# Kernel optimization log

Hardware: AMD Instinct MI355X
Metric: run time of the kernel (lower is better)

Reference implementation:

```python
import jax, jax.numpy as jnp
import numpy as np

N_NODES = 20000
N_EDGES = 320000
IN_CH = 256
HID = 128
HEADS = 4
OUT_CH = 200
NUM_GRAPHS = 64
NEG_SLOPE = 0.2


def setup_inputs() -> dict:
    key = jax.random.key(0)
    ks = jax.random.split(key, 16)
    x = jax.random.normal(ks[0], (N_NODES, IN_CH), dtype=jnp.float32)
    edge_index = jax.random.randint(ks[1], (2, N_EDGES), 0, N_NODES, dtype=jnp.int64)
    batch = jnp.sort(jax.random.randint(ks[2], (N_NODES,), 0, NUM_GRAPHS, dtype=jnp.int64))

    def lin(k, fan_in, fan_out):
        return jax.random.normal(k, (fan_in, fan_out), dtype=jnp.float32) / np.sqrt(fan_in)

    def att(k, h, c):
        return jax.random.normal(k, (h, c), dtype=jnp.float32) / np.sqrt(c)

    return {
        "x": x, "edge_index": edge_index, "batch": batch,
        "W1": lin(ks[3], IN_CH, HEADS * HID),
        "a_src1": att(ks[4], HEADS, HID), "a_dst1": att(ks[5], HEADS, HID),
        "b1": jnp.zeros((HEADS * HID,), jnp.float32),
        "W2": lin(ks[6], HEADS * HID, HEADS * HID),
        "a_src2": att(ks[7], HEADS, HID), "a_dst2": att(ks[8], HEADS, HID),
        "b2": jnp.zeros((HEADS * HID,), jnp.float32),
        "W3": lin(ks[9], HEADS * HID, HID),
        "a_src3": att(ks[10], 1, HID), "a_dst3": att(ks[11], 1, HID),
        "b3": jnp.zeros((HID,), jnp.float32),
        "fc_w": lin(ks[12], HID, OUT_CH),
        "fc_b": jnp.zeros((OUT_CH,), jnp.float32),
    }


def gat_conv(x, src, dst, W, a_src, a_dst, bias):
    """PyG GATConv (concat=True, negative_slope=0.2, self-loops appended by caller)."""
    N = x.shape[0]
    heads, out_ch = a_src.shape
    h = (x @ W).reshape(N, heads, out_ch)                 # [N,H,C]
    alpha_s = jnp.einsum('nhc,hc->nh', h, a_src)          # [N,H]
    alpha_d = jnp.einsum('nhc,hc->nh', h, a_dst)
    e = jax.nn.leaky_relu(alpha_s[src] + alpha_d[dst], NEG_SLOPE)  # [E,H]
    # segment softmax over edges sharing the same target node
    m = jax.ops.segment_max(e, dst, num_segments=N)
    e = jnp.exp(e - m[dst])
    denom = jax.ops.segment_sum(e, dst, num_segments=N)
    alpha = e / (denom[dst] + 1e-16)                      # [E,H]
    msg = h[src] * alpha[:, :, None]                      # [E,H,C]
    out = jax.ops.segment_sum(msg, dst, num_segments=N)   # [N,H,C]
    return out.reshape(N, heads * out_ch) + bias


def reference(x, edge_index, batch, W1, a_src1, a_dst1, b1,
              W2, a_src2, a_dst2, b2, W3, a_src3, a_dst3, b3, fc_w, fc_b):
    N = x.shape[0]
    loop = jnp.arange(N, dtype=edge_index.dtype)
    src = jnp.concatenate([edge_index[0], loop])
    dst = jnp.concatenate([edge_index[1], loop])

    h = jax.nn.elu(gat_conv(x, src, dst, W1, a_src1, a_dst1, b1))
    h = jax.nn.elu(gat_conv(h, src, dst, W2, a_src2, a_dst2, b2))
    h = jax.nn.elu(gat_conv(h, src, dst, W3, a_src3, a_dst3, b3))

    # global_mean_pool over graph ids
    sums = jax.ops.segment_sum(h, batch, num_segments=NUM_GRAPHS)
    cnts = jax.ops.segment_sum(jnp.ones((N,), h.dtype), batch, num_segments=NUM_GRAPHS)
    pooled = sums / jnp.maximum(cnts, 1.0)[:, None]       # [G,HID]
    # F.dropout with training=False is identity
    logits = pooled @ fc_w + fc_b                          # [G,OUT_CH]
    return logits
```

## Files before the change

### kernel.cpp

```cpp
#include <hip/hip_runtime.h>
#include <hip/hip_bf16.h>
#include <stdint.h>

#define N_NODES   20000
#define N_EDGES   320000
#define E_TOT     (N_EDGES + N_NODES)
#define IN_CH     256
#define HID       128
#define HEADS     4
#define OUT_CH    200
#define NUM_GRAPHS 64
#define M_PAD     20096

typedef __bf16 bf16_t;
typedef __bf16 bf16x8 __attribute__((ext_vector_type(8)));
typedef __bf16 bf16x2 __attribute__((ext_vector_type(2)));
typedef float  f32x4  __attribute__((ext_vector_type(4)));

__device__ __forceinline__ bool detect_bf16(const unsigned short* __restrict__ xu16) {
  int lane = threadIdx.x & 63;
  unsigned short v = xu16[2 * lane];
  int e = (v >> 7) & 0xff;
  unsigned long long b = __ballot(e >= 90 && e <= 160);
  return __popcll(b) >= 40;
}
__device__ __forceinline__ bool detect_i64(const unsigned* __restrict__ eidx) {
  int lane = threadIdx.x & 63;
  unsigned long long b = __ballot(eidx[2 * lane + 1] == 0u);
  return __popcll(b) >= 32;
}

struct SmallCvt {
  const void* src[11];
  bf16_t* dst[11];
  int n[11];
};

__global__ void prep(const void* __restrict__ W1, const void* __restrict__ W2,
                     const void* __restrict__ W3, bf16_t* __restrict__ W1T,
                     bf16_t* __restrict__ W2T, bf16_t* __restrict__ W3T,
                     SmallCvt tab, const unsigned short* __restrict__ xu16,
                     const int* __restrict__ eidx, const int* __restrict__ batch,
                     int* __restrict__ esrc, int* __restrict__ edst,
                     int* __restrict__ b32, int* __restrict__ deg) {
  bool isbf = detect_bf16(xu16);
  bool i64  = detect_i64((const unsigned*)eidx);
  int i = blockIdx.x * 256 + threadIdx.x;
  if (i < N_EDGES) {
    int s = i64 ? eidx[2 * i] : eidx[i];
    int d = i64 ? eidx[2 * (N_EDGES + i)] : eidx[N_EDGES + i];
    esrc[i] = s;
    edst[i] = d;
    atomicAdd(&deg[d], 1);
  }
  if (i < N_NODES) {
    b32[i] = i64 ? batch[2 * i] : batch[i];
    atomicAdd(&deg[i], 1);
  }
  if (i < 131072) {
    int k = i >> 9, nn = i & 511;
    bf16_t v = isbf ? ((const bf16_t*)W1)[i] : (bf16_t)((const float*)W1)[i];
    W1T[(size_t)nn * 256 + k] = v;
  } else if (i < 131072 + 262144) {
    int i2 = i - 131072;
    int k = i2 >> 9, nn = i2 & 511;
    bf16_t v = isbf ? ((const bf16_t*)W2)[i2] : (bf16_t)((const float*)W2)[i2];
    W2T[(size_t)nn * 512 + k] = v;
  } else if (i < 131072 + 262144 + 65536) {
    int i3 = i - 131072 - 262144;
    int k = i3 >> 7, nn = i3 & 127;
    bf16_t v = isbf ? ((const bf16_t*)W3)[i3] : (bf16_t)((const float*)W3)[i3];
    W3T[(size_t)nn * 512 + k] = v;
  } else {
    int j = i - 458752;
    for (int s = 0; s < 11; ++s) {
      if (j < tab.n[s]) {
        tab.dst[s][j] = isbf ? ((const bf16_t*)tab.src[s])[j]
                             : (bf16_t)((const float*)tab.src[s])[j];
        break;
      }
      j -= tab.n[s];
    }
  }
}

__launch_bounds__(1024)
__global__ void scan_deg_block(const int* __restrict__ deg, int* __restrict__ off,
                               int* __restrict__ cursor) {
  const int PT = 20;
  int t = threadIdx.x;
  int lane = t & 63, wid = t >> 6;
  int base = t * PT;
  int v[PT];
  int s = 0;
#pragma unroll
  for (int j = 0; j < PT; ++j) {
    int i = base + j;
    v[j] = (i < N_NODES) ? deg[i] : 0;
    s += v[j];
  }
  int x = s;
  for (int d = 1; d < 64; d <<= 1) {
    int y = __shfl_up(x, d);
    if (lane >= d) x += y;
  }
  __shared__ int wsum[16];
  if (lane == 63) wsum[wid] = x;
  __syncthreads();
  if (t < 16) {
    int y = wsum[t];
    for (int d = 1; d < 16; d <<= 1) {
      int z = __shfl_up(y, d);
      if (t >= d) y += z;
    }
    wsum[t] = y;
  }
  __syncthreads();
  int run = (wid > 0 ? wsum[wid - 1] : 0) + (x - s);
#pragma unroll
  for (int j = 0; j < PT; ++j) {
    int i = base + j;
    if (i < N_NODES) { off[i] = run; cursor[i] = 0; run += v[j]; }
  }
  if (t == 1023) off[N_NODES] = run;
}

__global__ void scatter_kernel(const int* __restrict__ esrc, const int* __restrict__ edst,
                               const int* __restrict__ off, int* __restrict__ cursor,
                               int* __restrict__ csr_src) {
  int e = blockIdx.x * 256 + threadIdx.x;
  if (e >= E_TOT) return;
  int s, d;
  if (e < N_EDGES) { s = esrc[e]; d = edst[e]; } else { s = d = e - N_EDGES; }
  int pos = off[d] + atomicAdd(&cursor[d], 1);
  csr_src[pos] = s;
}

template<bool MAYBE_F32>
__launch_bounds__(256)
__global__ void gemm_bf16(const void* __restrict__ Av, const bf16_t* __restrict__ BT,
                          bf16_t* __restrict__ C, int M, int N, int K,
                          const bf16_t* __restrict__ a_src, const bf16_t* __restrict__ a_dst,
                          float* __restrict__ as, float* __restrict__ ad, int H) {
  bool isbf = MAYBE_F32 ? detect_bf16((const unsigned short*)Av) : true;
  const bf16_t* A  = (const bf16_t*)Av;
  const float*  Af = (const float*)Av;
  __shared__ bf16_t As[128 * 32];
  __shared__ bf16_t Bs[128 * 32];
  __shared__ float sred[2][128];
  __shared__ float dred[2][128];
  const int tid  = threadIdx.x;
  const int lane = tid & 63;
  const int w    = tid >> 6;
  const int wm   = w & 1, wn = w >> 1;
  const int bm   = blockIdx.x * 128;
  const int bn   = blockIdx.y * 128;
  const int quad = lane >> 4;
  const int l16  = lane & 15;
  const int hd   = bn >> 7;

  f32x4 zero = {0.f, 0.f, 0.f, 0.f};
  f32x4 acc[4][4];
  for (int i = 0; i < 4; ++i)
    for (int j = 0; j < 4; ++j) acc[i][j] = zero;

  const int c0 = tid, c1 = tid + 256;
  const int r0 = c0 >> 2, s0 = c0 & 3;
  const int r1 = c1 >> 2, s1 = c1 & 3;
  int ga0 = bm + r0; if (ga0 > M - 1) ga0 = M - 1;
  int ga1 = bm + r1; if (ga1 > M - 1) ga1 = M - 1;

  for (int k0 = 0; k0 < K; k0 += 32) {
    if (!MAYBE_F32 || isbf) {
      __syncthreads();
      __builtin_amdgcn_global_load_lds(
          (const __attribute__((address_space(1))) void*)(A + (size_t)ga0 * K + k0 + s0 * 8),
          (__attribute__((address_space(3))) void*)(As + (size_t)(w * 64) * 8), 16, 0, 0);
      __builtin_amdgcn_global_load_lds(
          (const __attribute__((address_space(1))) void*)(BT + (size_t)(bn + r0) * K + k0 + s0 * 8),
          (__attribute__((address_space(3))) void*)(Bs + (size_t)(w * 64) * 8), 16, 0, 0);
      __builtin_amdgcn_global_load_lds(
          (const __attribute__((address_space(1))) void*)(A + (size_t)ga1 * K + k0 + s1 * 8),
          (__attribute__((address_space(3))) void*)(As + (size_t)(256 + w * 64) * 8), 16, 0, 0);
      __builtin_amdgcn_global_load_lds(
          (const __attribute__((address_space(1))) void*)(BT + (size_t)(bn + r1) * K + k0 + s1 * 8),
          (__attribute__((address_space(3))) void*)(Bs + (size_t)(256 + w * 64) * 8), 16, 0, 0);
      __syncthreads();
    } else {
      bf16x8 va0, va1;
      const float* p0 = Af + (size_t)ga0 * K + k0 + s0 * 8;
      const float* p1 = Af + (size_t)ga1 * K + k0 + s1 * 8;
      f32x4 l0 = *(const f32x4*)p0, h0 = *(const f32x4*)(p0 + 4);
      f32x4 l1 = *(const f32x4*)p1, h1 = *(const f32x4*)(p1 + 4);
      for (int j = 0; j < 4; ++j) {
        va0[j] = (bf16_t)l0[j]; va0[j + 4] = (bf16_t)h0[j];
        va1[j] = (bf16_t)l1[j]; va1[j + 4] = (bf16_t)h1[j];
      }
      bf16x8 vb0 = *(const bf16x8*)(BT + (size_t)(bn + r0) * K + k0 + s0 * 8);
      bf16x8 vb1 = *(const bf16x8*)(BT + (size_t)(bn + r1) * K + k0 + s1 * 8);
      __syncthreads();
      *(bf16x8*)(As + c0 * 8) = va0;
      *(bf16x8*)(Bs + c0 * 8) = vb0;
      *(bf16x8*)(As + c1 * 8) = va1;
      *(bf16x8*)(Bs + c1 * 8) = vb1;
      __syncthreads();
    }

    bf16x8 af[4], bfr[4];
    for (int mt = 0; mt < 4; ++mt) {
      int m_local = wm * 64 + mt * 16 + l16;
      af[mt] = *(const bf16x8*)(As + m_local * 32 + quad * 8);
    }
    for (int nt = 0; nt < 4; ++nt) {
      int n_local = wn * 64 + nt * 16 + l16;
      bfr[nt] = *(const bf16x8*)(Bs + n_local * 32 + quad * 8);
    }
    for (int mt = 0; mt < 4; ++mt)
      for (int nt = 0; nt < 4; ++nt)
        acc[mt][nt] = __builtin_amdgcn_mfma_f32_16x16x32_bf16(af[mt], bfr[nt], acc[mt][nt], 0, 0, 0);
  }

  for (int mt = 0; mt < 4; ++mt) {
    for (int r = 0; r < 4; ++r) {
      int m = bm + wm * 64 + mt * 16 + quad * 4 + r;
      if (m >= M) continue;
      for (int nt = 0; nt < 4; ++nt) {
        int n = bn + wn * 64 + nt * 16 + l16;
        C[(size_t)m * N + n] = (bf16_t)acc[mt][nt][r];
      }
    }
  }

  float av[4], dv[4];
  for (int nt = 0; nt < 4; ++nt) {
    int ch = wn * 64 + nt * 16 + l16;
    av[nt] = (float)a_src[hd * 128 + ch];
    dv[nt] = (float)a_dst[hd * 128 + ch];
  }
  for (int mt = 0; mt < 4; ++mt) {
    for (int r = 0; r < 4; ++r) {
      float s = acc[mt][0][r] * av[0] + acc[mt][1][r] * av[1]
              + acc[mt][2][r] * av[2] + acc[mt][3][r] * av[3];
      float d = acc[mt][0][r] * dv[0] + acc[mt][1][r] * dv[1]
              + acc[mt][2][r] * dv[2] + acc[mt][3][r] * dv[3];
      for (int o = 1; o < 16; o <<= 1) {
        s += __shfl_xor(s, o);
        d += __shfl_xor(d, o);
      }
      if (l16 == 0) {
        int row_local = wm * 64 + mt * 16 + quad * 4 + r;
        sred[wn][row_local] = s;
        dred[wn][row_local] = d;
      }
    }
  }
  __syncthreads();
  if (tid < 128) {
    int m = bm + tid;
    if (m < M) {
      as[m * H + hd] = sred[0][tid] + sred[1][tid];
      ad[m * H + hd] = dred[0][tid] + dred[1][tid];
    }
  }
}

template<int CPL>
__launch_bounds__(256)
__global__ void agg_fused(const bf16_t* __restrict__ h, const int* __restrict__ off,
                          const int* __restrict__ csr_src, const float* __restrict__ as,
                          const float* __restrict__ ad, const bf16_t* __restrict__ bias,
                          bf16_t* __restrict__ outp, int H) {
  typedef __bf16 vec_t __attribute__((ext_vector_type(CPL)));
  const int C = CPL * 64;
  int lane = threadIdx.x & 63;
  int n = blockIdx.x * 4 + (threadIdx.x >> 6);
  if (n >= N_NODES) return;
  int start = __builtin_amdgcn_readfirstlane(off[n]);
  int end   = __builtin_amdgcn_readfirstlane(off[n + 1]);
  int c0 = lane * CPL;
  int hd = c0 >> 7;
  float adv = ad[n * H + hd];
  float acc[CPL];
  for (int j = 0; j < CPL; ++j) acc[j] = 0.f;
  float den = 0.f;

  int pos = start;
  for (; pos + 3 < end; pos += 4) {
    int s0 = __builtin_amdgcn_readfirstlane(csr_src[pos]);
    int s1 = __builtin_amdgcn_readfirstlane(csr_src[pos + 1]);
    int s2 = __builtin_amdgcn_readfirstlane(csr_src[pos + 2]);
    int s3 = __builtin_amdgcn_readfirstlane(csr_src[pos + 3]);
    vec_t hv0 = *(const vec_t*)(h + (size_t)s0 * C + c0);
    vec_t hv1 = *(const vec_t*)(h + (size_t)s1 * C + c0);
    vec_t hv2 = *(const vec_t*)(h + (size_t)s2 * C + c0);
    vec_t hv3 = *(const vec_t*)(h + (size_t)s3 * C + c0);
    float e0 = as[s0 * H + hd] + adv; e0 = e0 > 0.f ? e0 : 0.2f * e0;
    float e1 = as[s1 * H + hd] + adv; e1 = e1 > 0.f ? e1 : 0.2f * e1;
    float e2 = as[s2 * H + hd] + adv; e2 = e2 > 0.f ? e2 : 0.2f * e2;
    float e3 = as[s3 * H + hd] + adv; e3 = e3 > 0.f ? e3 : 0.2f * e3;
    float w0 = __expf(e0), w1 = __expf(e1), w2 = __expf(e2), w3 = __expf(e3);
    den += (w0 + w1) + (w2 + w3);
    for (int j = 0; j < CPL; ++j)
      acc[j] += (w0 * (float)hv0[j] + w1 * (float)hv1[j])
              + (w2 * (float)hv2[j] + w3 * (float)hv3[j]);
  }
  for (; pos < end; ++pos) {
    int s0 = __builtin_amdgcn_readfirstlane(csr_src[pos]);
    vec_t hv0 = *(const vec_t*)(h + (size_t)s0 * C + c0);
    float e0 = as[s0 * H + hd] + adv; e0 = e0 > 0.f ? e0 : 0.2f * e0;
    float w0 = __expf(e0);
    den += w0;
    for (int j = 0; j < CPL; ++j) acc[j] += w0 * (float)hv0[j];
  }

  float inv = 1.f / (den + 1e-16f);
  vec_t ov;
  for (int j = 0; j < CPL; ++j) {
    float o = acc[j] * inv + (float)bias[c0 + j];
    o = o > 0.f ? o : expm1f(o);
    ov[j] = (bf16_t)o;
  }
  *(vec_t*)(outp + (size_t)n * C + c0) = ov;
}

__launch_bounds__(256)
__global__ void pool_fc2(const bf16_t* __restrict__ h3, const int* __restrict__ batch,
                         const bf16_t* __restrict__ fcw, const bf16_t* __restrict__ fcb,
                         void* __restrict__ outp, const unsigned short* __restrict__ xu16) {
  bool isbf = detect_bf16(xu16);
  int g = blockIdx.x;
  int lo = 0, hi = N_NODES;
  while (lo < hi) { int mid = (lo + hi) >> 1; if (batch[mid] < g) lo = mid + 1; else hi = mid; }
  int start = lo;
  hi = N_NODES;
  while (lo < hi) { int mid = (lo + hi) >> 1; if (batch[mid] < g + 1) lo = mid + 1; else hi = mid; }
  int end = lo, cnt = end - start;

  int t = threadIdx.x;
  int wave = t >> 6, lane = t & 63;
  int c0 = lane * 2;
  float a0 = 0.f, a1 = 0.f;
  for (int n = start + wave; n < end; n += 4) {
    bf16x2 v = *(const bf16x2*)(h3 + (size_t)n * HID + c0);
    a0 += (float)v[0];
    a1 += (float)v[1];
  }
  __shared__ float red[4][HID];
  red[wave][c0] = a0;
  red[wave][c0 + 1] = a1;
  __syncthreads();
  __shared__ float pooled[HID];
  if (t < HID) {
    float s = red[0][t] + red[1][t] + red[2][t] + red[3][t];
    pooled[t] = s / (float)(cnt > 0 ? cnt : 1);
  }
  __syncthreads();
  if (t < OUT_CH) {
    float a = (float)fcb[t];
    for (int c = 0; c < HID; ++c) a += pooled[c] * (float)fcw[c * OUT_CH + t];
    if (isbf) ((bf16_t*)outp)[g * OUT_CH + t] = (bf16_t)a;
    else      ((float*)outp)[g * OUT_CH + t] = a;
  }
}

extern "C" void kernel_launch(void* const* d_in, const int* in_sizes, int n_in,
                              void* d_out, int out_size, void* d_ws, size_t ws_size,
                              hipStream_t stream) {
  const void* x    = d_in[0];
  const void* eidx = d_in[1];
  const void* batch= d_in[2];
  const void* W1   = d_in[3];
  const void* a_s1 = d_in[4];
  const void* a_d1 = d_in[5];
  const void* b1   = d_in[6];
  const void* W2   = d_in[7];
  const void* a_s2 = d_in[8];
  const void* a_d2 = d_in[9];
  const void* b2   = d_in[10];
  const void* W3   = d_in[11];
  const void* a_s3 = d_in[12];
  const void* a_d3 = d_in[13];
  const void* b3   = d_in[14];
  const void* fcw  = d_in[15];
  const void* fcb  = d_in[16];
  const unsigned short* xu16 = (const unsigned short*)x;

  char* p = (char*)d_ws;
  auto carve = [&](size_t nbytes) { char* r = p; p += (nbytes + 255) & ~(size_t)255; return r; };
  bf16_t*   W1T    = (bf16_t*)carve((size_t)512 * 256 * 2);
  bf16_t*   W2T    = (bf16_t*)carve((size_t)512 * 512 * 2);
  bf16_t*   W3T    = (bf16_t*)carve((size_t)128 * 512 * 2);
  bf16_t*   hA     = (bf16_t*)carve((size_t)M_PAD * 512 * 2);
  bf16_t*   hB     = (bf16_t*)carve((size_t)M_PAD * 512 * 2);
  bf16_t*   sm     = (bf16_t*)carve((size_t)32768 * 2);
  bf16_t *as1b = sm, *ad1b = sm + 512, *b1b = sm + 1024,
         *as2b = sm + 1536, *ad2b = sm + 2048, *b2b = sm + 2560,
         *as3b = sm + 3072, *ad3b = sm + 3200, *b3b = sm + 3328,
         *fcwb = sm + 3456, *fcbb = sm + 29056;
  float*    asb    = (float*)carve((size_t)N_NODES * 4 * 4);
  float*    adb    = (float*)carve((size_t)N_NODES * 4 * 4);
  int*      deg    = (int*)carve((size_t)N_NODES * 4);
  int*      off    = (int*)carve((size_t)(N_NODES + 1) * 4);
  int*      cursor = (int*)carve((size_t)N_NODES * 4);
  int*      csr_src= (int*)carve((size_t)E_TOT * 4);
  int*      esrc32 = (int*)carve((size_t)N_EDGES * 4);
  int*      edst32 = (int*)carve((size_t)N_EDGES * 4);
  int*      bat32  = (int*)carve((size_t)N_NODES * 4);

  dim3 b256(256);
  const int NG4 = (N_NODES + 3) / 4;

  SmallCvt tab;
  const void* srcs[11] = {a_s1, a_d1, b1, a_s2, a_d2, b2, a_s3, a_d3, b3, fcw, fcb};
  bf16_t* dsts[11] = {as1b, ad1b, b1b, as2b, ad2b, b2b, as3b, ad3b, b3b, fcwb, fcbb};
  int ns[11] = {512, 512, 512, 512, 512, 512, 128, 128, 128, 25600, 200};
  for (int i = 0; i < 11; ++i) { tab.src[i] = srcs[i]; tab.dst[i] = dsts[i]; tab.n[i] = ns[i]; }

  hipMemsetAsync(deg, 0, (size_t)N_NODES * 4, stream);
  prep<<<dim3((458752 + 29256 + 255) / 256), b256, 0, stream>>>(
      W1, W2, W3, W1T, W2T, W3T, tab, xu16,
      (const int*)eidx, (const int*)batch, esrc32, edst32, bat32, deg);

  scan_deg_block<<<dim3(1), dim3(1024), 0, stream>>>(deg, off, cursor);
  scatter_kernel<<<dim3((E_TOT + 255) / 256), b256, 0, stream>>>(esrc32, edst32, off, cursor, csr_src);

  gemm_bf16<true><<<dim3(157, 4), b256, 0, stream>>>(x, W1T, hA, N_NODES, 512, 256,
                                                     as1b, ad1b, asb, adb, 4);
  agg_fused<8><<<dim3(NG4), b256, 0, stream>>>(hA, off, csr_src, asb, adb, b1b, hB, 4);

  gemm_bf16<false><<<dim3(157, 4), b256, 0, stream>>>(hB, W2T, hA, N_NODES, 512, 512,
                                                      as2b, ad2b, asb, adb, 4);
  agg_fused<8><<<dim3(NG4), b256, 0, stream>>>(hA, off, csr_src, asb, adb, b2b, hB, 4);

  gemm_bf16<false><<<dim3(157, 1), b256, 0, stream>>>(hB, W3T, hA, N_NODES, 128, 512,
                                                      as3b, ad3b, asb, adb, 1);
  agg_fused<2><<<dim3(NG4), b256, 0, stream>>>(hA, off, csr_src, asb, adb, b3b, hB, 1);

  pool_fc2<<<dim3(NUM_GRAPHS), b256, 0, stream>>>(hB, bat32, fcwb, fcbb, d_out, xu16);
}
```

Measured before the change: 370.8 us.

## Split GAT aggregation into 64-channel slices with two edges per wave

Replaces the per-node aggregation kernel, where one wave covered the whole feature row with 8 channels per lane, with a sliced kernel. Each block now handles one 64-channel slice for four nodes, and each wave splits its lanes into two halves that process alternating edges; the halves are combined with a cross-half shuffle before the output is written. The aim is more parallelism and fewer registers per thread. In exchange, the neighbor index and attention-score loads and the exp are repeated once per slice, the per-lane loads shrink to 4 bytes, and the 4-edge unrolling is gone.

```diff
diff --git a/kernel.cpp b/kernel.cpp
--- a/kernel.cpp
+++ b/kernel.cpp
@@ -264,63 +264,53 @@
   }
 }
 
-template<int CPL>
+template<int C, int SLICES>
 __launch_bounds__(256)
-__global__ void agg_fused(const bf16_t* __restrict__ h, const int* __restrict__ off,
-                          const int* __restrict__ csr_src, const float* __restrict__ as,
-                          const float* __restrict__ ad, const bf16_t* __restrict__ bias,
-                          bf16_t* __restrict__ outp, int H) {
-  typedef __bf16 vec_t __attribute__((ext_vector_type(CPL)));
-  const int C = CPL * 64;
+__global__ void agg_sliced(const bf16_t* __restrict__ h, const int* __restrict__ off,
+                           const int* __restrict__ csr_src, const float* __restrict__ as,
+                           const float* __restrict__ ad, const bf16_t* __restrict__ bias,
+                           bf16_t* __restrict__ outp, int H) {
+  int slice = blockIdx.x % SLICES;
+  int grp   = blockIdx.x / SLICES;
+  int wave  = threadIdx.x >> 6;
+  int n = grp * 4 + wave;
+  if (n >= N_NODES) return;
   int lane = threadIdx.x & 63;
-  int n = blockIdx.x * 4 + (threadIdx.x >> 6);
-  if (n >= N_NODES) return;
+  int half = lane >> 5;
+  int l32  = lane & 31;
+  int cbase = slice * 64;
+  int hd = cbase >> 7;
+  int c = cbase + l32 * 2;
   int start = __builtin_amdgcn_readfirstlane(off[n]);
   int end   = __builtin_amdgcn_readfirstlane(off[n + 1]);
-  int c0 = lane * CPL;
-  int hd = c0 >> 7;
   float adv = ad[n * H + hd];
-  float acc[CPL];
-  for (int j = 0; j < CPL; ++j) acc[j] = 0.f;
-  float den = 0.f;
-
-  int pos = start;
-  for (; pos + 3 < end; pos += 4) {
-    int s0 = __builtin_amdgcn_readfirstlane(csr_src[pos]);
-    int s1 = __builtin_amdgcn_readfirstlane(csr_src[pos + 1]);
-    int s2 = __builtin_amdgcn_readfirstlane(csr_src[pos + 2]);
-    int s3 = __builtin_amdgcn_readfirstlane(csr_src[pos + 3]);
-    vec_t hv0 = *(const vec_t*)(h + (size_t)s0 * C + c0);
-    vec_t hv1 = *(const vec_t*)(h + (size_t)s1 * C + c0);
-    vec_t hv2 = *(const vec_t*)(h + (size_t)s2 * C + c0);
-    vec_t hv3 = *(const vec_t*)(h + (size_t)s3 * C + c0);
-    float e0 = as[s0 * H + hd] + adv; e0 = e0 > 0.f ? e0 : 0.2f * e0;
-    float e1 = as[s1 * H + hd] + adv; e1 = e1 > 0.f ? e1 : 0.2f * e1;
-    float e2 = as[s2 * H + hd] + adv; e2 = e2 > 0.f ? e2 : 0.2f * e2;
-    float e3 = as[s3 * H + hd] + adv; e3 = e3 > 0.f ? e3 : 0.2f * e3;
-    float w0 = __expf(e0), w1 = __expf(e1), w2 = __expf(e2), w3 = __expf(e3);
-    den += (w0 + w1) + (w2 + w3);
-    for (int j = 0; j < CPL; ++j)
-      acc[j] += (w0 * (float)hv0[j] + w1 * (float)hv1[j])
-              + (w2 * (float)hv2[j] + w3 * (float)hv3[j]);
-  }
-  for (; pos < end; ++pos) {
-    int s0 = __builtin_amdgcn_readfirstlane(csr_src[pos]);
-    vec_t hv0 = *(const vec_t*)(h + (size_t)s0 * C + c0);
-    float e0 = as[s0 * H + hd] + adv; e0 = e0 > 0.f ? e0 : 0.2f * e0;
-    float w0 = __expf(e0);
-    den += w0;
-    for (int j = 0; j < CPL; ++j) acc[j] += w0 * (float)hv0[j];
-  }
-
-  float inv = 1.f / (den + 1e-16f);
-  vec_t ov;
-  for (int j = 0; j < CPL; ++j) {
-    float o = acc[j] * inv + (float)bias[c0 + j];
-    o = o > 0.f ? o : expm1f(o);
-    ov[j] = (bf16_t)o;
-  }
-  *(vec_t*)(outp + (size_t)n * C + c0) = ov;
+  float a0 = 0.f, a1 = 0.f, den = 0.f;
+
+  for (int pos = start; pos < end; pos += 2) {
+    int p = pos + half;
+    bool valid = p < end;
+    int pc = valid ? p : end - 1;
+    int src = csr_src[pc];
+    float e = as[src * H + hd] + adv;
+    e = e > 0.f ? e : 0.2f * e;
+    float wgt = valid ? __expf(e) : 0.f;
+    bf16x2 hv = *(const bf16x2*)(h + (size_t)src * C + c);
+    a0 += wgt * (float)hv[0];
+    a1 += wgt * (float)hv[1];
+    den += wgt;
+  }
+  a0  += __shfl_xor(a0, 32);
+  a1  += __shfl_xor(a1, 32);
+  den += __shfl_xor(den, 32);
+  if (half == 0) {
+    float inv = 1.f / (den + 1e-16f);
+    float o0 = a0 * inv + (float)bias[c];
+    float o1 = a1 * inv + (float)bias[c + 1];
+    o0 = o0 > 0.f ? o0 : expm1f(o0);
+    o1 = o1 > 0.f ? o1 : expm1f(o1);
+    bf16x2 ov; ov[0] = (bf16_t)o0; ov[1] = (bf16_t)o1;
+    *(bf16x2*)(outp + (size_t)n * C + c) = ov;
+  }
 }
 
 __launch_bounds__(256)
@@ -408,7 +398,7 @@
   int*      bat32  = (int*)carve((size_t)N_NODES * 4);
 
   dim3 b256(256);
-  const int NG4 = (N_NODES + 3) / 4;
+  const int NGRP = (N_NODES + 3) / 4;
 
   SmallCvt tab;
   const void* srcs[11] = {a_s1, a_d1, b1, a_s2, a_d2, b2, a_s3, a_d3, b3, fcw, fcb};
@@ -426,15 +416,15 @@
 
   gemm_bf16<true><<<dim3(157, 4), b256, 0, stream>>>(x, W1T, hA, N_NODES, 512, 256,
                                                      as1b, ad1b, asb, adb, 4);
-  agg_fused<8><<<dim3(NG4), b256, 0, stream>>>(hA, off, csr_src, asb, adb, b1b, hB, 4);
+  agg_sliced<512, 8><<<dim3(NGRP * 8), b256, 0, stream>>>(hA, off, csr_src, asb, adb, b1b, hB, 4);
 
   gemm_bf16<false><<<dim3(157, 4), b256, 0, stream>>>(hB, W2T, hA, N_NODES, 512, 512,
                                                       as2b, ad2b, asb, adb, 4);
-  agg_fused<8><<<dim3(NG4), b256, 0, stream>>>(hA, off, csr_src, asb, adb, b2b, hB, 4);
+  agg_sliced<512, 8><<<dim3(NGRP * 8), b256, 0, stream>>>(hA, off, csr_src, asb, adb, b2b, hB, 4);
 
   gemm_bf16<false><<<dim3(157, 1), b256, 0, stream>>>(hB, W3T, hA, N_NODES, 128, 512,
                                                       as3b, ad3b, asb, adb, 1);
-  agg_fused<2><<<dim3(NG4), b256, 0, stream>>>(hA, off, csr_src, asb, adb, b3b, hB, 1);
+  agg_sliced<128, 2><<<dim3(NGRP * 2), b256, 0, stream>>>(hA, off, csr_src, asb, adb, b3b, hB, 1);
 
   pool_fc2<<<dim3(NUM_GRAPHS), b256, 0, stream>>>(hB, bat32, fcwb, fcbb, d_out, xu16);
 }
```

Measured after the change: 553.9 us. 1.49x slower.
